# Kernel tuning notes

Measured on AMD Instinct MI355X. Metric: run time of the kernel, lower is better.

The kernel has to match this reference:

```python
import jax, jax.numpy as jnp
import numpy as np

B, N, F_IN, F_OUT = 8, 4096, 256, 256


def setup_inputs() -> dict:
    key = jax.random.key(0)
    k1, k2, k3 = jax.random.split(key, 3)
    H = jax.random.normal(k1, (B, N, F_IN), dtype=jnp.float32)
    W = jax.random.normal(k2, (F_IN, F_OUT), dtype=jnp.float32) * (1.0 / np.sqrt(F_IN))
    A = jax.random.normal(k3, (N, N), dtype=jnp.float32) * (1.414 * np.sqrt(2.0 / (N + N)))
    return {"H": H, "W": W, "A": A}


def reference(H, W, A):
    # HW: [B, N, F_out]
    HW = jnp.einsum('bnf,fo->bno', H, W)
    # symmetrize + relu -> nonneg adjacency [N, N]
    A_norm = jax.nn.relu((A + A.T) * 0.5)
    # degree and inverse sqrt (inf -> 0 for isolated nodes)
    D = jnp.sum(A_norm, axis=1)
    D_safe = jnp.where(D > 0, D, 1.0)
    d_inv_sqrt = jnp.where(D > 0, D_safe ** -0.5, 0.0)
    # L_norm = I - D^{-1/2} A D^{-1/2}  (diagonal scaling, no dense diag matmul)
    DAD = d_inv_sqrt[:, None] * A_norm * d_inv_sqrt[None, :]
    L_norm = jnp.eye(N, dtype=H.dtype) - DAD
    # output = relu(L_norm @ HW): [B, N, F_out]
    out = jnp.einsum('nm,bmo->bno', L_norm, HW)
    return jax.nn.relu(out)
```

## Files before the change

kernel.cpp:

```cpp
#include <hip/hip_runtime.h>
#include <stdint.h>

#define N_NODES 4096
#define F_DIM   256
#define BATCH   8

typedef __attribute__((ext_vector_type(8))) __bf16 bf16x8;
typedef __attribute__((ext_vector_type(4))) float  f32x4;
typedef __attribute__((ext_vector_type(8))) unsigned short u16x8;

typedef const __attribute__((address_space(1))) void* gas1_t;
typedef __attribute__((address_space(3))) void*       las3_t;

__device__ __forceinline__ void stage16(const void* g, void* l) {
  __builtin_amdgcn_global_load_lds((gas1_t)g, (las3_t)l, 16, 0, 0);
}

__device__ __forceinline__ unsigned short f2bf(float f) {
  union { float f; uint32_t u; } v; v.f = f;
  uint32_t u = v.u;
  return (unsigned short)((u + 0x7FFFu + ((u >> 16) & 1u)) >> 16);
}
__device__ __forceinline__ float bf2f(unsigned short u) {
  union { uint32_t u; float f; } v; v.u = ((uint32_t)u) << 16;
  return v.f;
}

__global__ __launch_bounds__(256) void k_pre(const float* __restrict__ A,
                                             unsigned short* __restrict__ Sb,
                                             float* __restrict__ D,
                                             const float4* __restrict__ H4,
                                             ushort4* __restrict__ Hb4,
                                             const float* __restrict__ W,
                                             unsigned short* __restrict__ Wt) {
  int t = threadIdx.x;
  int bid = blockIdx.y * 64 + blockIdx.x;
  {
    int i = bid * 512 + t;
    float4 v = H4[i];
    ushort4 o; o.x = f2bf(v.x); o.y = f2bf(v.y); o.z = f2bf(v.z); o.w = f2bf(v.w);
    Hb4[i] = o;
    i += 256;
    v = H4[i];
    o.x = f2bf(v.x); o.y = f2bf(v.y); o.z = f2bf(v.z); o.w = f2bf(v.w);
    Hb4[i] = o;
  }
  if (bid < 256) Wt[t * 256 + bid] = f2bf(W[bid * 256 + t]);

  int bi = blockIdx.y, bj = blockIdx.x;
  if (bj < bi) return;
  __shared__ float L1[64][65];
  __shared__ float L2[64][65];
  __shared__ float Pr[4][64];
  __shared__ float Pc[4][64];
  int i0 = bi * 64, j0 = bj * 64;
  for (int it = 0; it < 16; ++it) {
    int idx = it * 256 + t;
    int r = idx >> 6, c = idx & 63;
    L1[r][c] = A[(size_t)(i0 + r) * N_NODES + (j0 + c)];
    L2[c][r] = A[(size_t)(j0 + r) * N_NODES + (i0 + c)];
  }
  __syncthreads();
  float colsum = 0.f;
  int cfix = t & 63, q = t >> 6;
  for (int it = 0; it < 16; ++it) {
    int r = it * 4 + q;
    float v = 0.5f * (L1[r][cfix] + L2[r][cfix]);
    v = v > 0.f ? v : 0.f;
    Sb[(size_t)(i0 + r) * N_NODES + (j0 + cfix)] = f2bf(v);
    colsum += v;
    L1[r][cfix] = v;
  }
  Pc[q][cfix] = colsum;
  __syncthreads();
  {
    int r = t & 63, seg = t >> 6;
    float s = 0.f;
    for (int c = seg * 16; c < seg * 16 + 16; ++c) s += L1[r][c];
    Pr[seg][r] = s;
  }
  __syncthreads();
  if (t < 64) {
    float d = Pr[0][t] + Pr[1][t] + Pr[2][t] + Pr[3][t];
    atomicAdd(&D[i0 + t], d);
  } else if (t < 128 && bi != bj) {
    int c = t - 64;
    float d = Pc[0][c] + Pc[1][c] + Pc[2][c] + Pc[3][c];
    atomicAdd(&D[j0 + c], d);
  }
  if (bi != bj) {
    for (int it = 0; it < 16; ++it) {
      int idx = it * 256 + t;
      int ro = idx >> 6, co = idx & 63;
      Sb[(size_t)(j0 + ro) * N_NODES + (i0 + co)] = f2bf(L1[co][ro]);
    }
  }
}

__global__ void k_dinv(const float* __restrict__ D, float* __restrict__ dinv) {
  int i = blockIdx.x * blockDim.x + threadIdx.x;
  if (i < N_NODES) {
    float d = D[i];
    dinv[i] = d > 0.f ? 1.0f / sqrtf(d) : 0.f;
  }
}

__global__ __launch_bounds__(256) void k_gemm1(const unsigned short* __restrict__ Hb,
                                               const unsigned short* __restrict__ Wt,
                                               const float* __restrict__ dinv,
                                               unsigned short* __restrict__ HWb,
                                               unsigned short* __restrict__ Gt) {
  __shared__ __align__(16) unsigned short As[128 * 32];
  __shared__ __align__(16) unsigned short Bs[128 * 32];
  __shared__ __align__(16) unsigned short T[128][136];
  int t = threadIdx.x;
  int lane = t & 63;
  int q = lane >> 4, r16 = lane & 15;
  int wave = t >> 6;
  int wm = wave >> 1, wn = wave & 1;
  int m0 = blockIdx.y * 128;
  int o0 = blockIdx.x * 128;
  const int K = 256;

  const unsigned short* Abase = Hb + (size_t)m0 * K;
  const unsigned short* Bbase = Wt + (size_t)o0 * K;

  f32x4 acc[4][4];
#pragma unroll
  for (int i = 0; i < 4; ++i)
#pragma unroll
    for (int j = 0; j < 4; ++j) acc[i][j] = f32x4{0.f, 0.f, 0.f, 0.f};

  int idx0 = t, idx1 = 256 + t;
  int wb0 = (t & ~63) * 8;
  int wb1 = (256 + (t & ~63)) * 8;

  for (int kt = 0; kt < K / 32; ++kt) {
    int kof = kt * 32;
    stage16(Abase + (size_t)(idx0 >> 2) * K + kof + ((idx0 & 3) << 3), &As[wb0]);
    stage16(Abase + (size_t)(idx1 >> 2) * K + kof + ((idx1 & 3) << 3), &As[wb1]);
    stage16(Bbase + (size_t)(idx0 >> 2) * K + kof + ((idx0 & 3) << 3), &Bs[wb0]);
    stage16(Bbase + (size_t)(idx1 >> 2) * K + kof + ((idx1 & 3) << 3), &Bs[wb1]);
    __syncthreads();
    bf16x8 a[4], b[4];
#pragma unroll
    for (int mi = 0; mi < 4; ++mi)
      a[mi] = *(const bf16x8*)&As[(wm * 64 + mi * 16 + r16) * 32 + q * 8];
#pragma unroll
    for (int ni = 0; ni < 4; ++ni)
      b[ni] = *(const bf16x8*)&Bs[(wn * 64 + ni * 16 + r16) * 32 + q * 8];
#pragma unroll
    for (int mi = 0; mi < 4; ++mi)
#pragma unroll
      for (int ni = 0; ni < 4; ++ni)
        acc[mi][ni] = __builtin_amdgcn_mfma_f32_16x16x32_bf16(a[mi], b[ni], acc[mi][ni], 0, 0, 0);
    __syncthreads();
  }

#pragma unroll
  for (int mi = 0; mi < 4; ++mi) {
    int row = wm * 64 + mi * 16 + q * 4;
#pragma unroll
    for (int ni = 0; ni < 4; ++ni) {
      int col = wn * 64 + ni * 16 + r16;
#pragma unroll
      for (int rr = 0; rr < 4; ++rr) {
        unsigned short h = f2bf(acc[mi][ni][rr]);
        HWb[(size_t)(m0 + row + rr) * F_DIM + (o0 + col)] = h;
        T[col][row + rr] = h;
      }
    }
  }
  __syncthreads();
  int b = m0 >> 12, n0 = m0 & 4095;
  for (int it = 0; it < 8; ++it) {
    int unit = it * 256 + t;
    int ro = unit >> 4;
    int cs = (unit & 15) * 8;
    u16x8 v = *(const u16x8*)&T[ro][cs];
    u16x8 w;
#pragma unroll
    for (int j = 0; j < 8; ++j)
      w[j] = f2bf(bf2f(v[j]) * dinv[n0 + cs + j]);
    *(u16x8*)&Gt[(size_t)(b * 256 + o0 + ro) * N_NODES + n0 + cs] = w;
  }
}

__global__ __launch_bounds__(256, 2) void k_gemm2(const unsigned short* __restrict__ Sb,
                                                  const unsigned short* __restrict__ Gt,
                                                  const unsigned short* __restrict__ HWb,
                                                  const float* __restrict__ dinv,
                                                  float* __restrict__ Out) {
  __shared__ __align__(16) unsigned short As[128 * 32];
  __shared__ __align__(16) unsigned short Bs[128 * 32];
  __shared__ float Red[64 * 130];
  const int K = N_NODES;
  int t = threadIdx.x;
  int lane = t & 63;
  int q = lane >> 4, r16 = lane & 15;
  int wave = t >> 6;
  int wm = wave >> 1;
  int kz = wave & 1;

  int bid = blockIdx.y * 16 + blockIdx.x;
  int patch = bid & 7;
  int local = bid >> 3;
  int mt = (patch >> 1) * 8 + (local & 7);
  int nt = (patch & 1) * 8 + (local >> 3);
  int m0 = mt * 128;
  int n0 = nt * 128;

  const unsigned short* Abase = Sb + (size_t)m0 * K;
  const unsigned short* Bbase = Gt + (size_t)n0 * K;

  f32x4 acc[4][8];
#pragma unroll
  for (int i = 0; i < 4; ++i)
#pragma unroll
    for (int j = 0; j < 8; ++j) acc[i][j] = f32x4{0.f, 0.f, 0.f, 0.f};

  int u0 = t, u1 = 256 + t;
  int r0 = u0 >> 2, q0 = ((u0 & 3) - (r0 >> 1)) & 3;
  int r1 = u1 >> 2, q1 = ((u1 & 3) - (r1 >> 1)) & 3;
  const unsigned short* pa0 = Abase + (size_t)r0 * K + q0 * 8;
  const unsigned short* pa1 = Abase + (size_t)r1 * K + q1 * 8;
  const unsigned short* pb0 = Bbase + (size_t)r0 * K + q0 * 8;
  const unsigned short* pb1 = Bbase + (size_t)r1 * K + q1 * 8;
  int wb0 = (t & ~63) * 8;
  int wb1 = (256 + (t & ~63)) * 8;

  int aoff[4], boff[8];
#pragma unroll
  for (int mi = 0; mi < 4; ++mi) {
    int row = wm * 64 + mi * 16 + r16;
    aoff[mi] = row * 32 + (((q + (row >> 1)) & 3) << 3);
  }
#pragma unroll
  for (int ni = 0; ni < 8; ++ni) {
    int row = ni * 16 + r16;
    boff[ni] = row * 32 + (((q + (row >> 1)) & 3) << 3);
  }

  for (int kt = 0; kt < K / 32; ++kt) {
    int kof = kt * 32;
    stage16(pa0 + kof, &As[wb0]);
    stage16(pa1 + kof, &As[wb1]);
    stage16(pb0 + kof, &Bs[wb0]);
    stage16(pb1 + kof, &Bs[wb1]);
    __syncthreads();
    if ((kt & 1) == kz) {
      bf16x8 a[4], b[8];
#pragma unroll
      for (int mi = 0; mi < 4; ++mi) a[mi] = *(const bf16x8*)&As[aoff[mi]];
#pragma unroll
      for (int ni = 0; ni < 8; ++ni) b[ni] = *(const bf16x8*)&Bs[boff[ni]];
#pragma unroll
      for (int mi = 0; mi < 4; ++mi)
#pragma unroll
        for (int ni = 0; ni < 8; ++ni)
          acc[mi][ni] = __builtin_amdgcn_mfma_f32_16x16x32_bf16(a[mi], b[ni], acc[mi][ni], 0, 0, 0);
    }
    __syncthreads();
  }

  for (int round = 0; round < 2; ++round) {
    if (wm == round && kz == 1) {
#pragma unroll
      for (int mi = 0; mi < 4; ++mi)
#pragma unroll
        for (int ni = 0; ni < 8; ++ni)
#pragma unroll
          for (int rr = 0; rr < 4; ++rr)
            Red[(mi * 16 + q * 4 + rr) * 130 + ni * 16 + r16] = acc[mi][ni][rr];
    }
    __syncthreads();
    if (wm == round && kz == 0) {
#pragma unroll
      for (int mi = 0; mi < 4; ++mi) {
        int row = m0 + wm * 64 + mi * 16 + q * 4;
        float di[4];
#pragma unroll
        for (int rr = 0; rr < 4; ++rr) di[rr] = dinv[row + rr];
#pragma unroll
        for (int ni = 0; ni < 8; ++ni) {
          int col = n0 + ni * 16 + r16;
          int b_ = col >> 8, o = col & 255;
#pragma unroll
          for (int rr = 0; rr < 4; ++rr) {
            float v = acc[mi][ni][rr] + Red[(mi * 16 + q * 4 + rr) * 130 + ni * 16 + r16];
            size_t oi = ((size_t)b_ * N_NODES + (row + rr)) * F_DIM + o;
            float u = bf2f(HWb[oi]) - di[rr] * v;
            Out[oi] = u > 0.f ? u : 0.f;
          }
        }
      }
    }
    __syncthreads();
  }
}

extern "C" void kernel_launch(void* const* d_in, const int* in_sizes, int n_in,
                              void* d_out, int out_size, void* d_ws, size_t ws_size,
                              hipStream_t stream) {
  (void)in_sizes; (void)n_in; (void)out_size; (void)ws_size;
  const float* H = (const float*)d_in[0];
  const float* W = (const float*)d_in[1];
  const float* A = (const float*)d_in[2];
  float* out = (float*)d_out;

  char* ws = (char*)d_ws;
  size_t off = 0;
  auto alloc = [&](size_t bytes) {
    char* p = ws + off;
    off += (bytes + 255) & ~(size_t)255;
    return p;
  };
  float*          Dd   = (float*)alloc((size_t)N_NODES * 4);
  float*          dinv = (float*)alloc((size_t)N_NODES * 4);
  unsigned short* Sb   = (unsigned short*)alloc((size_t)N_NODES * N_NODES * 2);
  unsigned short* HWb  = (unsigned short*)alloc((size_t)BATCH * N_NODES * F_DIM * 2);
  unsigned short* Gt   = (unsigned short*)alloc((size_t)BATCH * F_DIM * N_NODES * 2);
  unsigned short* Wt   = (unsigned short*)alloc((size_t)F_DIM * F_DIM * 2);
  unsigned short* Hb   = (unsigned short*)alloc((size_t)BATCH * N_NODES * F_DIM * 2);

  hipMemsetAsync(Dd, 0, N_NODES * 4, stream);
  k_pre<<<dim3(64, 64), 256, 0, stream>>>(A, Sb, Dd, (const float4*)H, (ushort4*)Hb, W, Wt);
  k_dinv<<<16, 256, 0, stream>>>(Dd, dinv);
  k_gemm1<<<dim3(2, 256), 256, 0, stream>>>(Hb, Wt, dinv, HWb, Gt);
  k_gemm2<<<dim3(16, 32), 256, 0, stream>>>(Sb, Gt, HWb, dinv, out);
}
```

Baseline: 257.2 us.

## Rewrite main GEMM with 256x128 tiles, triple-buffered LDS pipeline, 8 waves

Replaces the 128x128 tile, split-K-across-waves GEMM with 256x128 tiles computed by 8 waves in a 4x2 layout. K steps are 64 wide and staged through a three-stage LDS ring using async global-to-LDS loads issued two tiles ahead, with a partial vmcnt wait and one barrier per step. This removes the second sync per k-step, the idle half of the waves, and the LDS reduction in the epilogue, and uses an XOR swizzle to avoid bank conflicts. The cost is 144KB of LDS per block, which may limit occupancy, and only 256 blocks are launched.

New measurement: 216.9 us. 15.7% less time.

```diff
diff --git a/kernel.cpp b/kernel.cpp
--- a/kernel.cpp
+++ b/kernel.cpp
@@ -186,116 +186,149 @@
   }
 }
 
-__global__ __launch_bounds__(256, 2) void k_gemm2(const unsigned short* __restrict__ Sb,
+#define LDSB 49152
+
+__global__ __launch_bounds__(512, 2) void k_gemm2(const unsigned short* __restrict__ Sb,
                                                   const unsigned short* __restrict__ Gt,
                                                   const unsigned short* __restrict__ HWb,
                                                   const float* __restrict__ dinv,
                                                   float* __restrict__ Out) {
-  __shared__ __align__(16) unsigned short As[128 * 32];
-  __shared__ __align__(16) unsigned short Bs[128 * 32];
-  __shared__ float Red[64 * 130];
-  const int K = N_NODES;
+  __shared__ __align__(16) unsigned short LDS[3 * 24576];
+  const int NT = N_NODES / 64;
   int t = threadIdx.x;
-  int lane = t & 63;
-  int q = lane >> 4, r16 = lane & 15;
+  int lane = t & 63, r16 = lane & 15, q = lane >> 4;
   int wave = t >> 6;
-  int wm = wave >> 1;
-  int kz = wave & 1;
-
-  int bid = blockIdx.y * 16 + blockIdx.x;
-  int patch = bid & 7;
-  int local = bid >> 3;
-  int mt = (patch >> 1) * 8 + (local & 7);
-  int nt = (patch & 1) * 8 + (local >> 3);
-  int m0 = mt * 128;
-  int n0 = nt * 128;
-
-  const unsigned short* Abase = Sb + (size_t)m0 * K;
-  const unsigned short* Bbase = Gt + (size_t)n0 * K;
-
-  f32x4 acc[4][8];
+  int wm = wave >> 1, wn = wave & 1;
+
+  int bid = blockIdx.x;
+  int xcd = bid & 7, j = bid >> 3;
+  int mt = (xcd >> 1) * 4 + (j & 3);
+  int nt = (xcd & 1) * 8 + (j >> 2);
+  int m0 = mt * 256, n0 = nt * 128;
+
+  const char* aSrc[4]; const char* bSrc[2];
+  uint32_t aDst[4], bDst[2];
+#pragma unroll
+  for (int i = 0; i < 4; ++i) {
+    int slot = i * 512 + t;
+    int row = slot >> 3;
+    int c = (slot & 7) ^ (row & 7);
+    aSrc[i] = (const char*)Sb + (size_t)(m0 + row) * 8192 + c * 16;
+    aDst[i] = (uint32_t)(i * 512 + (t & ~63)) * 16;
+  }
+#pragma unroll
+  for (int i = 0; i < 2; ++i) {
+    int slot = i * 512 + t;
+    int row = slot >> 3;
+    int c = (slot & 7) ^ (row & 7);
+    bSrc[i] = (const char*)Gt + (size_t)(n0 + row) * 8192 + c * 16;
+    bDst[i] = 32768u + (uint32_t)(i * 512 + (t & ~63)) * 16;
+  }
+
+  int aoff[4][2], boff[4][2];
+#pragma unroll
+  for (int mi = 0; mi < 4; ++mi) {
+    int ra = wm * 64 + mi * 16 + r16;
+#pragma unroll
+    for (int ks = 0; ks < 2; ++ks)
+      aoff[mi][ks] = ra * 128 + (((ks * 4 + q) ^ (ra & 7)) << 4);
+  }
+#pragma unroll
+  for (int ni = 0; ni < 4; ++ni) {
+    int rb = wn * 64 + ni * 16 + r16;
+#pragma unroll
+    for (int ks = 0; ks < 2; ++ks)
+      boff[ni][ks] = 32768 + rb * 128 + (((ks * 4 + q) ^ (rb & 7)) << 4);
+  }
+
+  f32x4 acc[4][4];
 #pragma unroll
   for (int i = 0; i < 4; ++i)
 #pragma unroll
-    for (int j = 0; j < 8; ++j) acc[i][j] = f32x4{0.f, 0.f, 0.f, 0.f};
-
-  int u0 = t, u1 = 256 + t;
-  int r0 = u0 >> 2, q0 = ((u0 & 3) - (r0 >> 1)) & 3;
-  int r1 = u1 >> 2, q1 = ((u1 & 3) - (r1 >> 1)) & 3;
-  const unsigned short* pa0 = Abase + (size_t)r0 * K + q0 * 8;
-  const unsigned short* pa1 = Abase + (size_t)r1 * K + q1 * 8;
-  const unsigned short* pb0 = Bbase + (size_t)r0 * K + q0 * 8;
-  const unsigned short* pb1 = Bbase + (size_t)r1 * K + q1 * 8;
-  int wb0 = (t & ~63) * 8;
-  int wb1 = (256 + (t & ~63)) * 8;
-
-  int aoff[4], boff[8];
+    for (int jj = 0; jj < 4; ++jj) acc[i][jj] = f32x4{0.f, 0.f, 0.f, 0.f};
+
+  auto stage_tile = [&](int kt2, uint32_t bufByte) {
+    size_t kb = (size_t)kt2 * 128;
+#pragma unroll
+    for (int i = 0; i < 4; ++i)
+      stage16(aSrc[i] + kb, (char*)LDS + bufByte + aDst[i]);
+#pragma unroll
+    for (int i = 0; i < 2; ++i)
+      stage16(bSrc[i] + kb, (char*)LDS + bufByte + bDst[i]);
+  };
+
+  auto tile_body = [&](int kt, uint32_t cur, int mode) {
+    bf16x8 aR[4][2], bR[4][2];
+#pragma unroll
+    for (int mi = 0; mi < 4; ++mi)
+#pragma unroll
+      for (int ks = 0; ks < 2; ++ks)
+        aR[mi][ks] = *(const bf16x8*)((const char*)LDS + cur + aoff[mi][ks]);
+#pragma unroll
+    for (int ni = 0; ni < 4; ++ni)
+#pragma unroll
+      for (int ks = 0; ks < 2; ++ks)
+        bR[ni][ks] = *(const bf16x8*)((const char*)LDS + cur + boff[ni][ks]);
+    if (mode == 2) {
+      uint32_t stg = cur + 2 * LDSB;
+      if (stg >= 3 * LDSB) stg -= 3 * LDSB;
+      stage_tile(kt + 2, stg);
+    }
+    __builtin_amdgcn_sched_barrier(0);
+    __builtin_amdgcn_s_setprio(1);
+#pragma unroll
+    for (int ks = 0; ks < 2; ++ks)
+#pragma unroll
+      for (int mi = 0; mi < 4; ++mi)
+#pragma unroll
+        for (int ni = 0; ni < 4; ++ni)
+          acc[mi][ni] = __builtin_amdgcn_mfma_f32_16x16x32_bf16(aR[mi][ks], bR[ni][ks], acc[mi][ni], 0, 0, 0);
+    __builtin_amdgcn_s_setprio(0);
+    if (mode == 2) {
+      asm volatile("s_waitcnt vmcnt(6)" ::: "memory");
+    } else if (mode == 1) {
+      asm volatile("s_waitcnt vmcnt(0)" ::: "memory");
+    }
+    if (mode != 0) {
+      __builtin_amdgcn_s_barrier();
+      __builtin_amdgcn_sched_barrier(0);
+    }
+  };
+
+  stage_tile(0, 0);
+  stage_tile(1, LDSB);
+  asm volatile("s_waitcnt vmcnt(6)" ::: "memory");
+  __builtin_amdgcn_s_barrier();
+  __builtin_amdgcn_sched_barrier(0);
+
+  uint32_t cur = 0;
+#pragma unroll 1
+  for (int kt = 0; kt < NT - 2; ++kt) {
+    tile_body(kt, cur, 2);
+    cur += LDSB; if (cur == 3 * LDSB) cur = 0;
+  }
+  tile_body(NT - 2, cur, 1);
+  cur += LDSB; if (cur == 3 * LDSB) cur = 0;
+  tile_body(NT - 1, cur, 0);
+
+  int bq = n0 >> 8;
 #pragma unroll
   for (int mi = 0; mi < 4; ++mi) {
-    int row = wm * 64 + mi * 16 + r16;
-    aoff[mi] = row * 32 + (((q + (row >> 1)) & 3) << 3);
-  }
-#pragma unroll
-  for (int ni = 0; ni < 8; ++ni) {
-    int row = ni * 16 + r16;
-    boff[ni] = row * 32 + (((q + (row >> 1)) & 3) << 3);
-  }
-
-  for (int kt = 0; kt < K / 32; ++kt) {
-    int kof = kt * 32;
-    stage16(pa0 + kof, &As[wb0]);
-    stage16(pa1 + kof, &As[wb1]);
-    stage16(pb0 + kof, &Bs[wb0]);
-    stage16(pb1 + kof, &Bs[wb1]);
-    __syncthreads();
-    if ((kt & 1) == kz) {
-      bf16x8 a[4], b[8];
-#pragma unroll
-      for (int mi = 0; mi < 4; ++mi) a[mi] = *(const bf16x8*)&As[aoff[mi]];
-#pragma unroll
-      for (int ni = 0; ni < 8; ++ni) b[ni] = *(const bf16x8*)&Bs[boff[ni]];
-#pragma unroll
-      for (int mi = 0; mi < 4; ++mi)
-#pragma unroll
-        for (int ni = 0; ni < 8; ++ni)
-          acc[mi][ni] = __builtin_amdgcn_mfma_f32_16x16x32_bf16(a[mi], b[ni], acc[mi][ni], 0, 0, 0);
-    }
-    __syncthreads();
-  }
-
-  for (int round = 0; round < 2; ++round) {
-    if (wm == round && kz == 1) {
-#pragma unroll
-      for (int mi = 0; mi < 4; ++mi)
-#pragma unroll
-        for (int ni = 0; ni < 8; ++ni)
-#pragma unroll
-          for (int rr = 0; rr < 4; ++rr)
-            Red[(mi * 16 + q * 4 + rr) * 130 + ni * 16 + r16] = acc[mi][ni][rr];
-    }
-    __syncthreads();
-    if (wm == round && kz == 0) {
-#pragma unroll
-      for (int mi = 0; mi < 4; ++mi) {
-        int row = m0 + wm * 64 + mi * 16 + q * 4;
-        float di[4];
-#pragma unroll
-        for (int rr = 0; rr < 4; ++rr) di[rr] = dinv[row + rr];
-#pragma unroll
-        for (int ni = 0; ni < 8; ++ni) {
-          int col = n0 + ni * 16 + r16;
-          int b_ = col >> 8, o = col & 255;
-#pragma unroll
-          for (int rr = 0; rr < 4; ++rr) {
-            float v = acc[mi][ni][rr] + Red[(mi * 16 + q * 4 + rr) * 130 + ni * 16 + r16];
-            size_t oi = ((size_t)b_ * N_NODES + (row + rr)) * F_DIM + o;
-            float u = bf2f(HWb[oi]) - di[rr] * v;
-            Out[oi] = u > 0.f ? u : 0.f;
-          }
-        }
+    int row = m0 + wm * 64 + mi * 16 + q * 4;
+    float di[4];
+#pragma unroll
+    for (int rr = 0; rr < 4; ++rr) di[rr] = dinv[row + rr];
+#pragma unroll
+    for (int ni = 0; ni < 4; ++ni) {
+      int col = n0 + wn * 64 + ni * 16 + r16;
+      int o = col & 255;
+#pragma unroll
+      for (int rr = 0; rr < 4; ++rr) {
+        size_t oi = ((size_t)bq * N_NODES + (row + rr)) * F_DIM + o;
+        float u = bf2f(HWb[oi]) - di[rr] * acc[mi][ni][rr];
+        Out[oi] = u > 0.f ? u : 0.f;
       }
     }
-    __syncthreads();
   }
 }
 
@@ -327,5 +360,5 @@
   k_pre<<<dim3(64, 64), 256, 0, stream>>>(A, Sb, Dd, (const float4*)H, (ushort4*)Hb, W, Wt);
   k_dinv<<<16, 256, 0, stream>>>(Dd, dinv);
   k_gemm1<<<dim3(2, 256), 256, 0, stream>>>(Hb, Wt, dinv, HWb, Gt);
-  k_gemm2<<<dim3(16, 32), 256, 0, stream>>>(Sb, Gt, HWb, dinv, out);
-}
+  k_gemm2<<<dim3(256), 512, 0, stream>>>(Sb, Gt, HWb, dinv, out);
+}
```
